# Optimization experiments

Hardware: AMD Instinct MI355X
Metric: run time of the kernel (lower is better)

## Reference

```python
import jax, jax.numpy as jnp
import numpy as np
from jax.scipy.special import logsumexp

EXPERT_NUM = 64
MOE_TOPK = 2

def setup_inputs() -> dict:
    key = jax.random.key(0)
    k1, k2 = jax.random.split(key)
    x = jax.random.normal(k1, (4, 4096, 4096), dtype=jnp.float32)
    # nn.Linear(input_size, expert_num).weight has shape [expert_num, input_size]
    W = jax.random.normal(k2, (EXPERT_NUM, 4096), dtype=jnp.float32) * (1.0 / np.sqrt(4096))
    return {"x": x, "W": W}

def reference(x, W):
    # logits: [B, S, E]
    logits = jnp.einsum('bsd,ed->bse', x, W)
    k = min(MOE_TOPK + 1, EXPERT_NUM)  # torch takes topk+1 then slices
    topk_logits, topk_indices = jax.lax.top_k(logits, k)
    topk_logits = topk_logits[..., :MOE_TOPK]     # [B, S, K]
    topk_indices = topk_indices[..., :MOE_TOPK]   # [B, S, K]
    # regularized=True: softmax over the top-k logits in float32
    topk_scores = jax.nn.softmax(topk_logits.astype(jnp.float32), axis=-1).astype(logits.dtype)
    # scatter into zeros; topk indices are unique so one-hot sum == scatter-set
    scores_filtered = jnp.sum(
        jax.nn.one_hot(topk_indices, EXPERT_NUM, dtype=logits.dtype) * topk_scores[..., None],
        axis=-2)  # [B, S, E]
    # router_z loss, per-token [B, S]
    log_z = logsumexp(logits, axis=-1)
    loss = log_z ** 2
    return logits, scores_filtered, loss
```

## Files before the change

### kernel.cpp

```cpp
#include <hip/hip_runtime.h>
#include <math.h>

#define TTOK 16384
#define DD   4096
#define EE   64
#define TMB  32
#define KW   1024
#define NIT  (KW / 32)
#define PST  68

typedef __attribute__((ext_vector_type(8))) short short8;
typedef __attribute__((ext_vector_type(4))) float f32x4;

static __device__ __forceinline__ unsigned short f2bf(float f) {
    unsigned u = __float_as_uint(f);
    u += 0x7FFFu + ((u >> 16) & 1u);
    return (unsigned short)(u >> 16);
}
static __device__ __forceinline__ float bf2f(unsigned short h) {
    return __uint_as_float(((unsigned)h) << 16);
}

static __device__ __forceinline__ void cvt8(float4 a, float4 b, short8& hi, short8& lo) {
    const float v[8] = {a.x, a.y, a.z, a.w, b.x, b.y, b.z, b.w};
#pragma unroll
    for (int j = 0; j < 8; ++j) {
        const unsigned short h = f2bf(v[j]);
        hi[j] = (short)h;
        lo[j] = (short)f2bf(v[j] - bf2f(h));
    }
}

__global__ void w_convert(const float* __restrict__ W,
                          unsigned short* __restrict__ whi,
                          unsigned short* __restrict__ wlo) {
    const int i = (blockIdx.x * blockDim.x + threadIdx.x) * 4;
    if (i >= EE * DD) return;
    const float4 v = *reinterpret_cast<const float4*>(W + i);
    ushort4 h, l;
    h.x = f2bf(v.x); l.x = f2bf(v.x - bf2f(h.x));
    h.y = f2bf(v.y); l.y = f2bf(v.y - bf2f(h.y));
    h.z = f2bf(v.z); l.z = f2bf(v.z - bf2f(h.z));
    h.w = f2bf(v.w); l.w = f2bf(v.w - bf2f(h.w));
    *reinterpret_cast<ushort4*>(whi + i) = h;
    *reinterpret_cast<ushort4*>(wlo + i) = l;
}

__global__ __launch_bounds__(256, 2)
void moe_gate_v3(const float* __restrict__ x,
                 const unsigned short* __restrict__ whi,
                 const unsigned short* __restrict__ wlo,
                 float* __restrict__ out)
{
    __shared__ float ps[4 * TMB * PST];
    __shared__ float s1a[TMB], s2a[TMB];
    __shared__ int   i1a[TMB], i2a[TMB];

    const int tid  = threadIdx.x;
    const int wv   = tid >> 6;
    const int lane = tid & 63;
    const int m    = lane & 15;
    const int q    = lane >> 4;
    const int t0   = blockIdx.x * TMB;

    const int kq = wv * KW + q * 8;
    const float*          xp0 = x   + (size_t)(t0 + m) * DD + kq;
    const float*          xp1 = xp0 + (size_t)16 * DD;
    const unsigned short* whp = whi + (size_t)m * DD + kq;
    const unsigned short* wlp = wlo + (size_t)m * DD + kq;

    f32x4 acc[2][4];
#pragma unroll
    for (int mi = 0; mi < 2; ++mi)
#pragma unroll
        for (int e = 0; e < 4; ++e) acc[mi][e] = (f32x4){0.f, 0.f, 0.f, 0.f};

    float4 a0 = *reinterpret_cast<const float4*>(xp0);
    float4 a1 = *reinterpret_cast<const float4*>(xp0 + 4);
    float4 a2 = *reinterpret_cast<const float4*>(xp1);
    float4 a3 = *reinterpret_cast<const float4*>(xp1 + 4);

    for (int it = 0; it < NIT; ++it) {
        float4 n0, n1, n2, n3;
        if (it + 1 < NIT) {
            const float* p0 = xp0 + (it + 1) * 32;
            const float* p1 = xp1 + (it + 1) * 32;
            n0 = *reinterpret_cast<const float4*>(p0);
            n1 = *reinterpret_cast<const float4*>(p0 + 4);
            n2 = *reinterpret_cast<const float4*>(p1);
            n3 = *reinterpret_cast<const float4*>(p1 + 4);
        }
        short8 ah0, al0, ah1, al1;
        cvt8(a0, a1, ah0, al0);
        cvt8(a2, a3, ah1, al1);
#pragma unroll
        for (int e = 0; e < 4; ++e) {
            const short8 bh = *reinterpret_cast<const short8*>(whp + (size_t)e * 16 * DD + it * 32);
            const short8 bl = *reinterpret_cast<const short8*>(wlp + (size_t)e * 16 * DD + it * 32);
            acc[0][e] = __builtin_amdgcn_mfma_f32_16x16x32_bf16(ah0, bh, acc[0][e], 0, 0, 0);
            acc[0][e] = __builtin_amdgcn_mfma_f32_16x16x32_bf16(ah0, bl, acc[0][e], 0, 0, 0);
            acc[0][e] = __builtin_amdgcn_mfma_f32_16x16x32_bf16(al0, bh, acc[0][e], 0, 0, 0);
            acc[1][e] = __builtin_amdgcn_mfma_f32_16x16x32_bf16(ah1, bh, acc[1][e], 0, 0, 0);
            acc[1][e] = __builtin_amdgcn_mfma_f32_16x16x32_bf16(ah1, bl, acc[1][e], 0, 0, 0);
            acc[1][e] = __builtin_amdgcn_mfma_f32_16x16x32_bf16(al1, bh, acc[1][e], 0, 0, 0);
        }
        a0 = n0; a1 = n1; a2 = n2; a3 = n3;
    }

#pragma unroll
    for (int mi = 0; mi < 2; ++mi)
#pragma unroll
        for (int e = 0; e < 4; ++e)
#pragma unroll
            for (int i = 0; i < 4; ++i)
                ps[wv * TMB * PST + (mi * 16 + 4 * q + i) * PST + 16 * e + m] = acc[mi][e][i];
    __syncthreads();

    {
        const int c0  = tid * 8;
        const int tok = c0 >> 6;
        const int e0  = c0 & 63;
        float* base = ps + tok * PST + e0;
        float4 s0 = *reinterpret_cast<const float4*>(base);
        float4 s1 = *reinterpret_cast<const float4*>(base + 4);
#pragma unroll
        for (int w = 1; w < 4; ++w) {
            const float4 r0 = *reinterpret_cast<const float4*>(base + w * TMB * PST);
            const float4 r1 = *reinterpret_cast<const float4*>(base + w * TMB * PST + 4);
            s0.x += r0.x; s0.y += r0.y; s0.z += r0.z; s0.w += r0.w;
            s1.x += r1.x; s1.y += r1.y; s1.z += r1.z; s1.w += r1.w;
        }
        float* g = out + (size_t)(t0 + tok) * EE + e0;
        *reinterpret_cast<float4*>(g)     = s0;
        *reinterpret_cast<float4*>(g + 4) = s1;
        *reinterpret_cast<float4*>(base)     = s0;
        *reinterpret_cast<float4*>(base + 4) = s1;
    }
    __syncthreads();

    if (tid < TMB) {
        const float* row = ps + tid * PST;
        float v1 = -INFINITY, v2 = -INFINITY;
        int   i1 = 0, i2 = 0;
        for (int e = 0; e < EE; ++e) {
            const float v = row[e];
            if (v > v1)      { v2 = v1; i2 = i1; v1 = v; i1 = e; }
            else if (v > v2) { v2 = v;  i2 = e; }
        }
        float s = 0.f;
        for (int e = 0; e < EE; ++e) s += expf(row[e] - v1);
        const float logz = v1 + logf(s);
        out[(size_t)2 * TTOK * EE + t0 + tid] = logz * logz;
        const float e21 = expf(v2 - v1);
        const float rr  = 1.f / (1.f + e21);
        s1a[tid] = rr; s2a[tid] = e21 * rr; i1a[tid] = i1; i2a[tid] = i2;
    }
    __syncthreads();

    {
        float* sc = out + (size_t)TTOK * EE;
        const int c0  = tid * 8;
        const int tok = c0 >> 6;
        const int e0  = c0 & 63;
        const int i1 = i1a[tok], i2 = i2a[tok];
        const float s1 = s1a[tok], s2 = s2a[tok];
        float vv[8];
#pragma unroll
        for (int j = 0; j < 8; ++j) {
            const int e = e0 + j;
            vv[j] = (e == i1) ? s1 : ((e == i2) ? s2 : 0.f);
        }
        float* g = sc + (size_t)(t0 + tok) * EE + e0;
        *reinterpret_cast<float4*>(g)     = make_float4(vv[0], vv[1], vv[2], vv[3]);
        *reinterpret_cast<float4*>(g + 4) = make_float4(vv[4], vv[5], vv[6], vv[7]);
    }
}

extern "C" void kernel_launch(void* const* d_in, const int* in_sizes, int n_in,
                              void* d_out, int out_size, void* d_ws, size_t ws_size,
                              hipStream_t stream) {
    const float* x = (const float*)d_in[0];
    const float* W = (const float*)d_in[1];
    float* out = (float*)d_out;
    unsigned short* whi = (unsigned short*)d_ws;
    unsigned short* wlo = whi + (size_t)EE * DD;
    w_convert<<<dim3((EE * DD / 4 + 255) / 256), dim3(256), 0, stream>>>(W, whi, wlo);
    moe_gate_v3<<<dim3(TTOK / TMB), dim3(256), 0, stream>>>(x, whi, wlo, out);
}
```

Before: 417.3 us.

## Split-K GEMM with async global-to-LDS staging and separate gate epilogue

Replaces the single fused kernel with a split-K GEMM that stages x and bf16 W tiles into XOR-swizzled LDS through global_load_lds async copies, then a separate epilogue kernel that sums the four K-slice partials and computes top-2 scores and the z-loss. Each block now covers 64 tokens and a quarter of K, so the per-wave cross-K reduction in LDS goes away and each W tile staged in LDS is reused across 64 tokens instead of every wave reading W directly from global memory. The cost is an extra partial buffer round-trip through global memory, an additional kernel launch, and two barriers per K-chunk with no double buffering.

```diff
diff --git a/kernel.cpp b/kernel.cpp
--- a/kernel.cpp
+++ b/kernel.cpp
@@ -4,10 +4,11 @@
 #define TTOK 16384
 #define DD   4096
 #define EE   64
-#define TMB  32
-#define KW   1024
-#define NIT  (KW / 32)
-#define PST  68
+#define TM   64
+#define BK   64
+#define KSL  4
+#define KW   (DD / KSL)
+#define NCHB (KW / BK)
 
 typedef __attribute__((ext_vector_type(8))) short short8;
 typedef __attribute__((ext_vector_type(4))) float f32x4;
@@ -19,6 +20,12 @@
 }
 static __device__ __forceinline__ float bf2f(unsigned short h) {
     return __uint_as_float(((unsigned)h) << 16);
+}
+
+static __device__ __forceinline__ void async16(const void* g, void* l) {
+    __builtin_amdgcn_global_load_lds(
+        (const __attribute__((address_space(1))) unsigned int*)g,
+        (__attribute__((address_space(3))) unsigned int*)l, 16, 0, 0);
 }
 
 static __device__ __forceinline__ void cvt8(float4 a, float4 b, short8& hi, short8& lo) {
@@ -46,100 +53,135 @@
     *reinterpret_cast<ushort4*>(wlo + i) = l;
 }
 
-__global__ __launch_bounds__(256, 2)
-void moe_gate_v3(const float* __restrict__ x,
-                 const unsigned short* __restrict__ whi,
-                 const unsigned short* __restrict__ wlo,
-                 float* __restrict__ out)
+__global__ __launch_bounds__(256, 4)
+void gemm_part(const float* __restrict__ x,
+               const unsigned short* __restrict__ whi,
+               const unsigned short* __restrict__ wlo,
+               float* __restrict__ part)
 {
-    __shared__ float ps[4 * TMB * PST];
-    __shared__ float s1a[TMB], s2a[TMB];
-    __shared__ int   i1a[TMB], i2a[TMB];
+    __shared__ float          xs[TM * 64];
+    __shared__ unsigned short whs[TM * 64];
+    __shared__ unsigned short wls[TM * 64];
 
     const int tid  = threadIdx.x;
     const int wv   = tid >> 6;
     const int lane = tid & 63;
     const int m    = lane & 15;
     const int q    = lane >> 4;
-    const int t0   = blockIdx.x * TMB;
-
-    const int kq = wv * KW + q * 8;
-    const float*          xp0 = x   + (size_t)(t0 + m) * DD + kq;
-    const float*          xp1 = xp0 + (size_t)16 * DD;
-    const unsigned short* whp = whi + (size_t)m * DD + kq;
-    const unsigned short* wlp = wlo + (size_t)m * DD + kq;
-
-    f32x4 acc[2][4];
-#pragma unroll
-    for (int mi = 0; mi < 2; ++mi)
-#pragma unroll
-        for (int e = 0; e < 4; ++e) acc[mi][e] = (f32x4){0.f, 0.f, 0.f, 0.f};
-
-    float4 a0 = *reinterpret_cast<const float4*>(xp0);
-    float4 a1 = *reinterpret_cast<const float4*>(xp0 + 4);
-    float4 a2 = *reinterpret_cast<const float4*>(xp1);
-    float4 a3 = *reinterpret_cast<const float4*>(xp1 + 4);
-
-    for (int it = 0; it < NIT; ++it) {
-        float4 n0, n1, n2, n3;
-        if (it + 1 < NIT) {
-            const float* p0 = xp0 + (it + 1) * 32;
-            const float* p1 = xp1 + (it + 1) * 32;
-            n0 = *reinterpret_cast<const float4*>(p0);
-            n1 = *reinterpret_cast<const float4*>(p0 + 4);
-            n2 = *reinterpret_cast<const float4*>(p1);
-            n3 = *reinterpret_cast<const float4*>(p1 + 4);
-        }
-        short8 ah0, al0, ah1, al1;
-        cvt8(a0, a1, ah0, al0);
-        cvt8(a2, a3, ah1, al1);
-#pragma unroll
-        for (int e = 0; e < 4; ++e) {
-            const short8 bh = *reinterpret_cast<const short8*>(whp + (size_t)e * 16 * DD + it * 32);
-            const short8 bl = *reinterpret_cast<const short8*>(wlp + (size_t)e * 16 * DD + it * 32);
-            acc[0][e] = __builtin_amdgcn_mfma_f32_16x16x32_bf16(ah0, bh, acc[0][e], 0, 0, 0);
-            acc[0][e] = __builtin_amdgcn_mfma_f32_16x16x32_bf16(ah0, bl, acc[0][e], 0, 0, 0);
-            acc[0][e] = __builtin_amdgcn_mfma_f32_16x16x32_bf16(al0, bh, acc[0][e], 0, 0, 0);
-            acc[1][e] = __builtin_amdgcn_mfma_f32_16x16x32_bf16(ah1, bh, acc[1][e], 0, 0, 0);
-            acc[1][e] = __builtin_amdgcn_mfma_f32_16x16x32_bf16(ah1, bl, acc[1][e], 0, 0, 0);
-            acc[1][e] = __builtin_amdgcn_mfma_f32_16x16x32_bf16(al1, bh, acc[1][e], 0, 0, 0);
-        }
-        a0 = n0; a1 = n1; a2 = n2; a3 = n3;
-    }
-
-#pragma unroll
-    for (int mi = 0; mi < 2; ++mi)
-#pragma unroll
-        for (int e = 0; e < 4; ++e)
-#pragma unroll
-            for (int i = 0; i < 4; ++i)
-                ps[wv * TMB * PST + (mi * 16 + 4 * q + i) * PST + 16 * e + m] = acc[mi][e][i];
+    const int tile = blockIdx.x & 255;
+    const int ks   = blockIdx.x >> 8;
+    const int t0   = tile * TM;
+    const int k0   = ks * KW;
+
+    const float* gx[4];
+#pragma unroll
+    for (int i = 0; i < 4; ++i) {
+        const int r = 16 * wv + 4 * i + q;
+        const int c = m ^ (r & 7);
+        gx[i] = x + (size_t)(t0 + r) * DD + k0 + c * 4;
+    }
+    const unsigned short* gwh[2];
+    const unsigned short* gwl[2];
+#pragma unroll
+    for (int i = 0; i < 2; ++i) {
+        const int r = 16 * wv + 8 * i + (lane >> 3);
+        const int c = (lane & 7) ^ (r & 7);
+        gwh[i] = whi + (size_t)r * DD + k0 + c * 8;
+        gwl[i] = wlo + (size_t)r * DD + k0 + c * 8;
+    }
+    float*          lx[4];
+    unsigned short* lwh[2];
+    unsigned short* lwl[2];
+#pragma unroll
+    for (int i = 0; i < 4; ++i) lx[i] = xs + wv * 1024 + i * 256;
+#pragma unroll
+    for (int i = 0; i < 2; ++i) {
+        lwh[i] = whs + wv * 1024 + i * 512;
+        lwl[i] = wls + wv * 1024 + i * 512;
+    }
+
+    f32x4 acc[4];
+#pragma unroll
+    for (int e = 0; e < 4; ++e) acc[e] = (f32x4){0.f, 0.f, 0.f, 0.f};
+
+    const int sa = m & 7;
+    const int ra = (16 * wv + m) * 64;
+
+    for (int kc = 0; kc < NCHB; ++kc) {
+        __syncthreads();
+#pragma unroll
+        for (int i = 0; i < 4; ++i) async16(gx[i] + kc * BK, lx[i]);
+#pragma unroll
+        for (int i = 0; i < 2; ++i) {
+            async16(gwh[i] + kc * BK, lwh[i]);
+            async16(gwl[i] + kc * BK, lwl[i]);
+        }
+        __syncthreads();
+
+#pragma unroll
+        for (int kss = 0; kss < 2; ++kss) {
+            const int c0 = 8 * kss + 2 * q;
+            const float4 f0 = *reinterpret_cast<const float4*>(xs + ra + ((c0    ) ^ sa) * 4);
+            const float4 f1 = *reinterpret_cast<const float4*>(xs + ra + ((c0 + 1) ^ sa) * 4);
+            short8 ah, al;
+            cvt8(f0, f1, ah, al);
+            const int pB = ((4 * kss + q) ^ sa) * 8;
+#pragma unroll
+            for (int e = 0; e < 4; ++e) {
+                const int rb = (16 * e + m) * 64;
+                const short8 bh = *reinterpret_cast<const short8*>(whs + rb + pB);
+                const short8 bl = *reinterpret_cast<const short8*>(wls + rb + pB);
+                acc[e] = __builtin_amdgcn_mfma_f32_16x16x32_bf16(ah, bh, acc[e], 0, 0, 0);
+                acc[e] = __builtin_amdgcn_mfma_f32_16x16x32_bf16(ah, bl, acc[e], 0, 0, 0);
+                acc[e] = __builtin_amdgcn_mfma_f32_16x16x32_bf16(al, bh, acc[e], 0, 0, 0);
+            }
+        }
+    }
+
+    float* pb = part + ((size_t)ks * TTOK + t0 + 16 * wv + 4 * q) * EE + m;
+#pragma unroll
+    for (int e = 0; e < 4; ++e)
+#pragma unroll
+        for (int i = 0; i < 4; ++i)
+            pb[(size_t)i * EE + 16 * e] = acc[e][i];
+}
+
+__global__ __launch_bounds__(256, 4)
+void gate_epi(const float* __restrict__ part, float* __restrict__ out)
+{
+    __shared__ float lg[TM * 68];
+    __shared__ float s1a[TM], s2a[TM];
+    __shared__ int   i1a[TM], i2a[TM];
+
+    const int tid = threadIdx.x;
+    const int t0  = blockIdx.x * TM;
+    const int tt  = tid >> 2;
+    const int e0  = (tid & 3) * 16;
+
+    const float* pbase = part + (size_t)(t0 + tt) * EE + e0;
+    float4 s[4];
+#pragma unroll
+    for (int j = 0; j < 4; ++j) s[j] = *reinterpret_cast<const float4*>(pbase + 4 * j);
+#pragma unroll
+    for (int k = 1; k < KSL; ++k) {
+        const float* pk = pbase + (size_t)k * TTOK * EE;
+#pragma unroll
+        for (int j = 0; j < 4; ++j) {
+            const float4 r = *reinterpret_cast<const float4*>(pk + 4 * j);
+            s[j].x += r.x; s[j].y += r.y; s[j].z += r.z; s[j].w += r.w;
+        }
+    }
+    float* g = out + (size_t)(t0 + tt) * EE + e0;
+    float* lrow = lg + tt * 68 + e0;
+#pragma unroll
+    for (int j = 0; j < 4; ++j) {
+        *reinterpret_cast<float4*>(g + 4 * j)    = s[j];
+        *reinterpret_cast<float4*>(lrow + 4 * j) = s[j];
+    }
     __syncthreads();
 
-    {
-        const int c0  = tid * 8;
-        const int tok = c0 >> 6;
-        const int e0  = c0 & 63;
-        float* base = ps + tok * PST + e0;
-        float4 s0 = *reinterpret_cast<const float4*>(base);
-        float4 s1 = *reinterpret_cast<const float4*>(base + 4);
-#pragma unroll
-        for (int w = 1; w < 4; ++w) {
-            const float4 r0 = *reinterpret_cast<const float4*>(base + w * TMB * PST);
-            const float4 r1 = *reinterpret_cast<const float4*>(base + w * TMB * PST + 4);
-            s0.x += r0.x; s0.y += r0.y; s0.z += r0.z; s0.w += r0.w;
-            s1.x += r1.x; s1.y += r1.y; s1.z += r1.z; s1.w += r1.w;
-        }
-        float* g = out + (size_t)(t0 + tok) * EE + e0;
-        *reinterpret_cast<float4*>(g)     = s0;
-        *reinterpret_cast<float4*>(g + 4) = s1;
-        *reinterpret_cast<float4*>(base)     = s0;
-        *reinterpret_cast<float4*>(base + 4) = s1;
-    }
-    __syncthreads();
-
-    if (tid < TMB) {
-        const float* row = ps + tid * PST;
+    if (tid < TM) {
+        const float* row = lg + tid * 68;
         float v1 = -INFINITY, v2 = -INFINITY;
         int   i1 = 0, i2 = 0;
         for (int e = 0; e < EE; ++e) {
@@ -147,9 +189,9 @@
             if (v > v1)      { v2 = v1; i2 = i1; v1 = v; i1 = e; }
             else if (v > v2) { v2 = v;  i2 = e; }
         }
-        float s = 0.f;
-        for (int e = 0; e < EE; ++e) s += expf(row[e] - v1);
-        const float logz = v1 + logf(s);
+        float sm = 0.f;
+        for (int e = 0; e < EE; ++e) sm += expf(row[e] - v1);
+        const float logz = v1 + logf(sm);
         out[(size_t)2 * TTOK * EE + t0 + tid] = logz * logz;
         const float e21 = expf(v2 - v1);
         const float rr  = 1.f / (1.f + e21);
@@ -157,22 +199,18 @@
     }
     __syncthreads();
 
-    {
-        float* sc = out + (size_t)TTOK * EE;
-        const int c0  = tid * 8;
-        const int tok = c0 >> 6;
-        const int e0  = c0 & 63;
-        const int i1 = i1a[tok], i2 = i2a[tok];
-        const float s1 = s1a[tok], s2 = s2a[tok];
-        float vv[8];
-#pragma unroll
-        for (int j = 0; j < 8; ++j) {
-            const int e = e0 + j;
-            vv[j] = (e == i1) ? s1 : ((e == i2) ? s2 : 0.f);
-        }
-        float* g = sc + (size_t)(t0 + tok) * EE + e0;
-        *reinterpret_cast<float4*>(g)     = make_float4(vv[0], vv[1], vv[2], vv[3]);
-        *reinterpret_cast<float4*>(g + 4) = make_float4(vv[4], vv[5], vv[6], vv[7]);
+    float* sc = out + (size_t)TTOK * EE + (size_t)(t0 + tt) * EE + e0;
+    const int i1 = i1a[tt], i2 = i2a[tt];
+    const float s1 = s1a[tt], s2 = s2a[tt];
+#pragma unroll
+    for (int j = 0; j < 4; ++j) {
+        float vv[4];
+#pragma unroll
+        for (int c = 0; c < 4; ++c) {
+            const int e = e0 + 4 * j + c;
+            vv[c] = (e == i1) ? s1 : ((e == i2) ? s2 : 0.f);
+        }
+        *reinterpret_cast<float4*>(sc + 4 * j) = make_float4(vv[0], vv[1], vv[2], vv[3]);
     }
 }
 
@@ -184,6 +222,9 @@
     float* out = (float*)d_out;
     unsigned short* whi = (unsigned short*)d_ws;
     unsigned short* wlo = whi + (size_t)EE * DD;
+    float* part = (float*)(wlo + (size_t)EE * DD);
+
     w_convert<<<dim3((EE * DD / 4 + 255) / 256), dim3(256), 0, stream>>>(W, whi, wlo);
-    moe_gate_v3<<<dim3(TTOK / TMB), dim3(256), 0, stream>>>(x, whi, wlo, out);
-}
+    gemm_part<<<dim3(256 * KSL), dim3(256), 0, stream>>>(x, whi, wlo, part);
+    gate_epi<<<dim3(TTOK / TM), dim3(256), 0, stream>>>(part, out);
+}
```

After: 399.6 us. 1.04x faster.
